# Optimization experiments

Hardware: AMD Instinct MI355X
Metric: run time of the kernel (lower is better)

## Reference

```python
import jax, jax.numpy as jnp
import numpy as np

HIDDEN = 896
NUM_Q_HEADS = 14
NUM_KV_HEADS = 2
HEAD_DIM = 64
ROPE_BASE = 10000.0
B, S = 4, 2048


def rotate_half(x):
    x1, x2 = jnp.split(x, 2, axis=-1)
    return jnp.concatenate((-x2, x1), axis=-1)


def rope_cos_sin(position_ids):
    # position_ids: [B, S] int -> cos/sin [B, 1, S, HEAD_DIM]
    inv_freq = 1.0 / (ROPE_BASE ** (jnp.arange(0, HEAD_DIM, 2, dtype=jnp.float32) / HEAD_DIM))
    freqs = position_ids.astype(jnp.float32)[..., None] * inv_freq  # [B,S,D/2]
    emb = jnp.concatenate((freqs, freqs), axis=-1)  # [B,S,D]
    return jnp.cos(emb)[:, None, :, :], jnp.sin(emb)[:, None, :, :]


def setup_inputs() -> dict:
    key = jax.random.key(0)
    k1, k2, k3, k4, k5 = jax.random.split(key, 5)
    s = 1.0 / np.sqrt(HIDDEN)
    return {
        "hidden_states": jax.random.normal(k1, (B, S, HIDDEN), dtype=jnp.float32),
        "position_ids": jnp.broadcast_to(jnp.arange(S, dtype=jnp.int64), (B, S)),
        "Wq": jax.random.normal(k2, (HIDDEN, NUM_Q_HEADS * HEAD_DIM), dtype=jnp.float32) * s,
        "Wk": jax.random.normal(k3, (HIDDEN, NUM_KV_HEADS * HEAD_DIM), dtype=jnp.float32) * s,
        "Wv": jax.random.normal(k4, (HIDDEN, NUM_KV_HEADS * HEAD_DIM), dtype=jnp.float32) * s,
        "Wo": jax.random.normal(k5, (NUM_Q_HEADS * HEAD_DIM, HIDDEN), dtype=jnp.float32) * s,
    }


def reference(hidden_states, position_ids, Wq, Wk, Wv, Wo):
    b, s, _ = hidden_states.shape
    n_rep = NUM_Q_HEADS // NUM_KV_HEADS

    q = (hidden_states @ Wq).reshape(b, s, NUM_Q_HEADS, HEAD_DIM).transpose(0, 2, 1, 3)   # [B,Hq,S,D]
    k = (hidden_states @ Wk).reshape(b, s, NUM_KV_HEADS, HEAD_DIM).transpose(0, 2, 1, 3)  # [B,Hkv,S,D]
    v = (hidden_states @ Wv).reshape(b, s, NUM_KV_HEADS, HEAD_DIM).transpose(0, 2, 1, 3)

    cos, sin = rope_cos_sin(position_ids)  # [B,1,S,D]
    q = q * cos + rotate_half(q) * sin
    k = k * cos + rotate_half(k) * sin

    # repeat_interleave KV heads to match query heads
    k = jnp.repeat(k, n_rep, axis=1)  # [B,Hq,S,D]
    v = jnp.repeat(v, n_rep, axis=1)

    scale = 1.0 / jnp.sqrt(jnp.float32(HEAD_DIM))
    attn = jnp.einsum('bhqd,bhkd->bhqk', q, k) * scale  # [B,Hq,S,S]
    attn = jax.nn.softmax(attn, axis=-1)
    out = jnp.einsum('bhqk,bhkd->bhqd', attn, v)  # [B,Hq,S,D]
    out = out.transpose(0, 2, 1, 3).reshape(b, s, NUM_Q_HEADS * HEAD_DIM)
    return out @ Wo
```

## Files before the change

### kernel.cpp

```cpp
#include <hip/hip_runtime.h>
#include <hip/hip_bf16.h>
#include <math.h>

typedef unsigned short ushort_t;
typedef __bf16 bf16x8 __attribute__((ext_vector_type(8)));
typedef float f32x4 __attribute__((ext_vector_type(4)));

#define HIDDEN 896
#define NQH 14
#define NKVH 2
#define HD 64
#define SEQ 2048
#define NBATCH 4

__device__ inline ushort_t f2bf(float x) {
  union { float f; unsigned u; } c; c.f = x;
  unsigned r = c.u + 0x7FFFu + ((c.u >> 16) & 1u);
  return (ushort_t)(r >> 16);
}

__device__ inline unsigned pack2bf(float a, float b) {
  union { float f; unsigned u; } ca, cb; ca.f = a; cb.f = b;
  unsigned ua = ca.u + 0x8000u, ub = cb.u + 0x8000u;
  return __builtin_amdgcn_perm(ub, ua, 0x07060302);
}

__device__ inline bf16x8 ldfrag(const ushort_t* p) {
  return *reinterpret_cast<const bf16x8*>(p);
}

__device__ inline void async16(const ushort_t* g, ushort_t* l) {
  __builtin_amdgcn_global_load_lds(
      (const __attribute__((address_space(1))) void*)g,
      (__attribute__((address_space(3))) void*)l, 16, 0, 0);
}


__device__ inline void transpose_sec(const float* __restrict__ in, ushort_t* __restrict__ out,
                                     int K, int N, int bx, int by) {
  __shared__ float tile[32][33];
  int k0 = by * 32, n0 = bx * 32;
  for (int r = threadIdx.y; r < 32; r += 8) {
    int k = k0 + r, n = n0 + threadIdx.x;
    tile[r][threadIdx.x] = (k < K && n < N) ? in[(size_t)k * N + n] : 0.f;
  }
  __syncthreads();
  for (int r = threadIdx.y; r < 32; r += 8) {
    int n = n0 + r, k = k0 + threadIdx.x;
    if (n < N && k < K) out[(size_t)n * K + k] = f2bf(tile[threadIdx.x][r]);
  }
}

__global__ void k_prep(const float* __restrict__ hidden, ushort_t* __restrict__ hb,
                       const float* __restrict__ Wq, const float* __restrict__ Wk,
                       const float* __restrict__ Wv, const float* __restrict__ Wo,
                       ushort_t* __restrict__ wT, ushort_t* __restrict__ woT,
                       float2* __restrict__ ctab) {
  const int blk = blockIdx.x;
  const int tid = threadIdx.y * 32 + threadIdx.x;
  if (blk < 7168) {
    int i = blk * 256 + tid;
    float4 v = reinterpret_cast<const float4*>(hidden)[i];
    ushort4 o;
    o.x = f2bf(v.x); o.y = f2bf(v.y); o.z = f2bf(v.z); o.w = f2bf(v.w);
    reinterpret_cast<ushort4*>(hb)[i] = o;
  } else if (blk < 7424) {
    int idx = (blk - 7168) * 256 + tid;
    int s = idx >> 5, dp = idx & 31;
    float inv = exp2f(-(float)dp * 0.41524101186092596f);
    float ang = (float)s * inv;
    float sn, cn;
    sincosf(ang, &sn, &cn);
    ctab[idx] = make_float2(cn, sn);
  } else if (blk < 8208) {
    int t = blk - 7424;
    transpose_sec(Wq, wT, 896, 896, t % 28, t / 28);
  } else if (blk < 8320) {
    int t = blk - 8208;
    transpose_sec(Wk, wT + (size_t)896 * 896, 896, 128, t % 4, t / 4);
  } else if (blk < 8432) {
    int t = blk - 8320;
    transpose_sec(Wv, wT + (size_t)1024 * 896, 896, 128, t % 4, t / 4);
  } else {
    int t = blk - 8432;
    transpose_sec(Wo, woT, 896, 896, t % 28, t / 28);
  }
}

__global__ __launch_bounds__(256) void k_qkv(
    const ushort_t* __restrict__ hb,
    const ushort_t* __restrict__ wT,
    const int* __restrict__ pos_ids,
    const float2* __restrict__ ctab,
    ushort_t* __restrict__ Qg,
    ushort_t* __restrict__ Kg,
    ushort_t* __restrict__ Vtg) {
  __shared__ ushort_t sa[128 * 32];
  __shared__ ushort_t sbb[128 * 32];

  const int f = blockIdx.x;
  const int x = f & 7, s8 = f >> 3;
  const int sect = s8 % 9;
  const int mt = (s8 / 9) * 8 + x;
  const int nt0 = sect * 128;
  const int m0 = mt * 128;
  const int tid = threadIdx.x;
  const int wave = tid >> 6, lane = tid & 63;
  const int l15 = lane & 15, quad = lane >> 4;
  const int wm = wave >> 1, wn = wave & 1;

  f32x4 acc[4][4];
  const f32x4 z4 = {0.f, 0.f, 0.f, 0.f};
#pragma unroll
  for (int a = 0; a < 4; ++a)
#pragma unroll
    for (int b = 0; b < 4; ++b) acc[a][b] = z4;

  for (int kt = 0; kt < 28; ++kt) {
    const int k0 = kt * 32;
    __syncthreads();
#pragma unroll
    for (int i = 0; i < 2; ++i) {
      int c = wave * 128 + i * 64 + lane;
      async16(hb + (size_t)(m0 + (c >> 2)) * HIDDEN + k0 + (c & 3) * 8,
              sa + (size_t)(wave * 128 + i * 64) * 8);
      async16(wT + (size_t)(nt0 + (c >> 2)) * HIDDEN + k0 + (c & 3) * 8,
              sbb + (size_t)(wave * 128 + i * 64) * 8);
    }
    __syncthreads();
    bf16x8 bf[4], af[4];
#pragma unroll
    for (int nb = 0; nb < 4; ++nb)
      bf[nb] = ldfrag(sbb + ((wn * 64 + nb * 16 + l15) * 32 + quad * 8));
#pragma unroll
    for (int mb = 0; mb < 4; ++mb)
      af[mb] = ldfrag(sa + ((wm * 64 + mb * 16 + l15) * 32 + quad * 8));
#pragma unroll
    for (int mb = 0; mb < 4; ++mb)
#pragma unroll
      for (int nb = 0; nb < 4; ++nb)
        acc[mb][nb] = __builtin_amdgcn_mfma_f32_16x16x32_bf16(af[mb], bf[nb], acc[mb][nb], 0, 0, 0);
  }

  if (sect < 8) {
    const bool isQ = sect < 7;
    const float csc = isQ ? 0.125f * 1.4426950408889634f : 1.0f;
    ushort_t* dst = isQ ? Qg : Kg;
    const int nheads = isQ ? NQH : NKVH;
    const int hh = isQ ? sect * 2 + wn : wn;
#pragma unroll
    for (int mb = 0; mb < 4; ++mb)
#pragma unroll
      for (int r = 0; r < 4; ++r) {
        int token = m0 + wm * 64 + mb * 16 + quad * 4 + r;
        int b = token >> 11, s = token & 2047;
        int pos = pos_ids[token];
        size_t base = ((size_t)(b * nheads + hh) * SEQ + s) * HD;
#pragma unroll
        for (int nb = 0; nb < 2; ++nb) {
          float2 cs = ctab[pos * 32 + nb * 16 + l15];
          float x0 = acc[mb][nb][r];
          float x1 = acc[mb][nb + 2][r];
          float y0 = (x0 * cs.x - x1 * cs.y) * csc;
          float y1 = (x1 * cs.x + x0 * cs.y) * csc;
          dst[base + nb * 16 + l15]      = f2bf(y0);
          dst[base + nb * 16 + l15 + 32] = f2bf(y1);
        }
      }
  } else {
#pragma unroll
    for (int mb = 0; mb < 4; ++mb) {
      int token0 = m0 + wm * 64 + mb * 16 + quad * 4;
      int b = token0 >> 11, s = token0 & 2047;
#pragma unroll
      for (int nb = 0; nb < 4; ++nb) {
        int d = nb * 16 + l15;
        uint2 pk;
        pk.x = pack2bf(acc[mb][nb][0], acc[mb][nb][1]);
        pk.y = pack2bf(acc[mb][nb][2], acc[mb][nb][3]);
        *reinterpret_cast<uint2*>(Vtg + ((size_t)(b * NKVH + wn) * HD + d) * SEQ + s) = pk;
      }
    }
  }
}

__global__ __launch_bounds__(256) void k_attn(
    const ushort_t* __restrict__ Qg,
    const ushort_t* __restrict__ Kg,
    const ushort_t* __restrict__ Vtg,
    ushort_t* __restrict__ attn) {
  __shared__ ushort_t kbuf[64 * 64];
  __shared__ ushort_t vbuf[64 * 64];
  __shared__ ushort_t pbuf[4][32 * 72];

  const int f = blockIdx.x;
  const int x = f & 7, s8 = f >> 3;
  const int lh = s8 >> 4;
  const int qt = s8 & 15;
  const int b = x >> 1, kvh = x & 1;
  const int h = kvh * 7 + lh;
  const int bh = b * NQH + h;
  const int tid = threadIdx.x;
  const int wave = tid >> 6, lane = tid & 63;
  const int l15 = lane & 15, quad = lane >> 4;
  const int q0 = qt * 128;

  bf16x8 qf[2][2];
#pragma unroll
  for (int qs = 0; qs < 2; ++qs) {
    const size_t qb = ((size_t)bh * SEQ + q0 + wave * 32 + qs * 16 + l15) * HD + quad * 8;
    qf[qs][0] = ldfrag(Qg + qb);
    qf[qs][1] = ldfrag(Qg + qb + 32);
  }

  bf16x8 ones;
#pragma unroll
  for (int i = 0; i < 8; ++i) ones[i] = (__bf16)1.0f;

  const size_t kbase = (size_t)(b * NKVH + kvh) * SEQ * HD;
  const size_t vbase = (size_t)(b * NKVH + kvh) * HD * SEQ;

  const int srow = tid >> 3;
  const int sc0 = (tid & 7) ^ (srow & 7);
  const int srow2 = (256 + tid) >> 3;
  const int sc2 = (tid & 7) ^ (srow2 & 7);
  const int sbase1 = wave * 64 * 8;
  const int sbase2 = (256 + wave * 64) * 8;

  f32x4 o[2][4];
  f32x4 lfr[2];
  const f32x4 z4 = {0.f, 0.f, 0.f, 0.f};
#pragma unroll
  for (int qs = 0; qs < 2; ++qs) {
    lfr[qs] = z4;
#pragma unroll
    for (int nb = 0; nb < 4; ++nb) o[qs][nb] = z4;
  }

  ushort_t* pw = pbuf[wave];

  for (int jt = 0; jt < 32; ++jt) {
    const int s0 = jt * 64;
    __syncthreads();
    async16(Kg + kbase + (size_t)(s0 + srow) * HD + sc0 * 8, kbuf + sbase1);
    async16(Vtg + vbase + (size_t)srow * SEQ + s0 + sc0 * 8, vbuf + sbase1);
    async16(Kg + kbase + (size_t)(s0 + srow2) * HD + sc2 * 8, kbuf + sbase2);
    async16(Vtg + vbase + (size_t)srow2 * SEQ + s0 + sc2 * 8, vbuf + sbase2);
    __syncthreads();

#pragma unroll
    for (int nb = 0; nb < 4; ++nb) {
      int row = nb * 16 + l15;
      int sw = row & 7;
      bf16x8 kf0 = ldfrag(kbuf + (row * 8 + (quad ^ sw)) * 8);
      bf16x8 kf1 = ldfrag(kbuf + (row * 8 + ((4 + quad) ^ sw)) * 8);
#pragma unroll
      for (int qs = 0; qs < 2; ++qs) {
        f32x4 t = z4;
        t = __builtin_amdgcn_mfma_f32_16x16x32_bf16(kf0, qf[qs][0], t, 0, 0, 0);
        t = __builtin_amdgcn_mfma_f32_16x16x32_bf16(kf1, qf[qs][1], t, 0, 0, 0);
        float p0 = __builtin_amdgcn_exp2f(t[0]);
        float p1 = __builtin_amdgcn_exp2f(t[1]);
        float p2 = __builtin_amdgcn_exp2f(t[2]);
        float p3 = __builtin_amdgcn_exp2f(t[3]);
        uint2 d;
        d.x = pack2bf(p0, p1);
        d.y = pack2bf(p2, p3);
        *reinterpret_cast<uint2*>(pw + (qs * 16 + l15) * 72 + nb * 16 + quad * 4) = d;
      }
    }

    bf16x8 pf[2][2];
#pragma unroll
    for (int qs = 0; qs < 2; ++qs) {
      pf[qs][0] = ldfrag(pw + (qs * 16 + l15) * 72 + quad * 8);
      pf[qs][1] = ldfrag(pw + (qs * 16 + l15) * 72 + 32 + quad * 8);
    }
#pragma unroll
    for (int qs = 0; qs < 2; ++qs) {
      lfr[qs] = __builtin_amdgcn_mfma_f32_16x16x32_bf16(pf[qs][0], ones, lfr[qs], 0, 0, 0);
      lfr[qs] = __builtin_amdgcn_mfma_f32_16x16x32_bf16(pf[qs][1], ones, lfr[qs], 0, 0, 0);
    }
#pragma unroll
    for (int nb = 0; nb < 4; ++nb) {
      int row = nb * 16 + l15;
      int sw = row & 7;
      bf16x8 vf0 = ldfrag(vbuf + (row * 8 + (quad ^ sw)) * 8);
      bf16x8 vf1 = ldfrag(vbuf + (row * 8 + ((4 + quad) ^ sw)) * 8);
#pragma unroll
      for (int qs = 0; qs < 2; ++qs) {
        o[qs][nb] = __builtin_amdgcn_mfma_f32_16x16x32_bf16(pf[qs][0], vf0, o[qs][nb], 0, 0, 0);
        o[qs][nb] = __builtin_amdgcn_mfma_f32_16x16x32_bf16(pf[qs][1], vf1, o[qs][nb], 0, 0, 0);
      }
    }
  }

#pragma unroll
  for (int qs = 0; qs < 2; ++qs) {
#pragma unroll
    for (int r = 0; r < 4; ++r) {
      float inv = 1.0f / lfr[qs][r];
      int qg = q0 + wave * 32 + qs * 16 + quad * 4 + r;
#pragma unroll
      for (int nb = 0; nb < 4; ++nb) {
        float val = o[qs][nb][r] * inv;
        attn[(size_t)(b * SEQ + qg) * (NQH * HD) + h * HD + nb * 16 + l15] = f2bf(val);
      }
    }
  }
}

__global__ __launch_bounds__(256) void k_oproj(
    const ushort_t* __restrict__ attn,
    const ushort_t* __restrict__ woT,
    float* __restrict__ out) {
  __shared__ ushort_t sa[128 * 32];
  __shared__ ushort_t sbb[128 * 32];

  const int f = blockIdx.x;
  const int x = f & 7, s8 = f >> 3;
  const int n_sect = s8 % 7;
  const int mt = (s8 / 7) * 8 + x;
  const int n0 = n_sect * 128;
  const int m0 = mt * 128;
  const int tid = threadIdx.x;
  const int wave = tid >> 6, lane = tid & 63;
  const int l15 = lane & 15, quad = lane >> 4;
  const int wm = wave >> 1, wn = wave & 1;

  f32x4 acc[4][4];
  const f32x4 z4 = {0.f, 0.f, 0.f, 0.f};
#pragma unroll
  for (int a = 0; a < 4; ++a)
#pragma unroll
    for (int b = 0; b < 4; ++b) acc[a][b] = z4;

  for (int kt = 0; kt < 28; ++kt) {
    const int k0 = kt * 32;
    __syncthreads();
#pragma unroll
    for (int i = 0; i < 2; ++i) {
      int c = wave * 128 + i * 64 + lane;
      async16(attn + (size_t)(m0 + (c >> 2)) * HIDDEN + k0 + (c & 3) * 8,
              sa + (size_t)(wave * 128 + i * 64) * 8);
      async16(woT + (size_t)(n0 + (c >> 2)) * HIDDEN + k0 + (c & 3) * 8,
              sbb + (size_t)(wave * 128 + i * 64) * 8);
    }
    __syncthreads();
    bf16x8 bf[4], af[4];
#pragma unroll
    for (int nb = 0; nb < 4; ++nb)
      bf[nb] = ldfrag(sbb + ((wn * 64 + nb * 16 + l15) * 32 + quad * 8));
#pragma unroll
    for (int mb = 0; mb < 4; ++mb)
      af[mb] = ldfrag(sa + ((wm * 64 + mb * 16 + l15) * 32 + quad * 8));
#pragma unroll
    for (int mb = 0; mb < 4; ++mb)
#pragma unroll
      for (int nb = 0; nb < 4; ++nb)
        acc[mb][nb] = __builtin_amdgcn_mfma_f32_16x16x32_bf16(af[mb], bf[nb], acc[mb][nb], 0, 0, 0);
  }

#pragma unroll
  for (int mb = 0; mb < 4; ++mb)
#pragma unroll
    for (int nb = 0; nb < 4; ++nb)
#pragma unroll
      for (int r = 0; r < 4; ++r)
        out[(size_t)(m0 + wm * 64 + mb * 16 + quad * 4 + r) * HIDDEN +
            n0 + wn * 64 + nb * 16 + l15] = acc[mb][nb][r];
}


extern "C" void kernel_launch(void* const* d_in, const int* in_sizes, int n_in,
                              void* d_out, int out_size, void* d_ws, size_t ws_size,
                              hipStream_t stream) {
  (void)in_sizes; (void)n_in; (void)out_size; (void)ws_size;
  const float* hidden = (const float*)d_in[0];
  const int* pos      = (const int*)d_in[1];
  const float* Wq     = (const float*)d_in[2];
  const float* Wk     = (const float*)d_in[3];
  const float* Wv     = (const float*)d_in[4];
  const float* Wo     = (const float*)d_in[5];
  float* out = (float*)d_out;

  char* ws = (char*)d_ws;
  ushort_t* hb   = (ushort_t*)(ws);
  ushort_t* wT   = (ushort_t*)(ws + 14680064);
  float2*   ctab = (float2*)  (ws + 16744448);
  ushort_t* Qg   = (ushort_t*)(ws + 17268736);
  ushort_t* Kg   = (ushort_t*)(ws + 31948800);
  ushort_t* Vtg  = (ushort_t*)(ws + 34045952);
  ushort_t* attn = (ushort_t*)(ws + 36143104);
  ushort_t* woT  = (ushort_t*)(ws + 50823168);

  k_prep<<<9216, dim3(32, 8), 0, stream>>>(hidden, hb, Wq, Wk, Wv, Wo, wT, woT, ctab);
  k_qkv<<<576, 256, 0, stream>>>(hb, wT, pos, ctab, Qg, Kg, Vtg);
  k_attn<<<896, 256, 0, stream>>>(Qg, Kg, Vtg, attn);
  k_oproj<<<448, 256, 0, stream>>>(attn, woT, out);
}
```

Measured before the change: 255.4 us.

## Widen GEMM K-tile with swizzled LDS, stage V transpose, enlarge attention query tile

Measured after the change: 277.4 us. +8.6%, slower.

```diff
diff --git a/kernel.cpp b/kernel.cpp
--- a/kernel.cpp
+++ b/kernel.cpp
@@ -95,8 +95,9 @@
     ushort_t* __restrict__ Qg,
     ushort_t* __restrict__ Kg,
     ushort_t* __restrict__ Vtg) {
-  __shared__ ushort_t sa[128 * 32];
-  __shared__ ushort_t sbb[128 * 32];
+  __shared__ ushort_t smem[16384];
+  ushort_t* sa = smem;
+  ushort_t* sbb = smem + 8192;
 
   const int f = blockIdx.x;
   const int x = f & 7, s8 = f >> 3;
@@ -108,6 +109,7 @@
   const int wave = tid >> 6, lane = tid & 63;
   const int l15 = lane & 15, quad = lane >> 4;
   const int wm = wave >> 1, wn = wave & 1;
+  const int sw = l15 & 7;
 
   f32x4 acc[4][4];
   const f32x4 z4 = {0.f, 0.f, 0.f, 0.f};
@@ -116,30 +118,37 @@
 #pragma unroll
     for (int b = 0; b < 4; ++b) acc[a][b] = z4;
 
-  for (int kt = 0; kt < 28; ++kt) {
-    const int k0 = kt * 32;
-    __syncthreads();
-#pragma unroll
-    for (int i = 0; i < 2; ++i) {
-      int c = wave * 128 + i * 64 + lane;
-      async16(hb + (size_t)(m0 + (c >> 2)) * HIDDEN + k0 + (c & 3) * 8,
-              sa + (size_t)(wave * 128 + i * 64) * 8);
-      async16(wT + (size_t)(nt0 + (c >> 2)) * HIDDEN + k0 + (c & 3) * 8,
-              sbb + (size_t)(wave * 128 + i * 64) * 8);
-    }
-    __syncthreads();
-    bf16x8 bf[4], af[4];
-#pragma unroll
-    for (int nb = 0; nb < 4; ++nb)
-      bf[nb] = ldfrag(sbb + ((wn * 64 + nb * 16 + l15) * 32 + quad * 8));
+  for (int kt = 0; kt < 14; ++kt) {
+    const int k0 = kt * 64;
+    __syncthreads();
+#pragma unroll
+    for (int i = 0; i < 4; ++i) {
+      int id = i * 256 + tid;
+      int row = id >> 3;
+      int cs = (id & 7) ^ (row & 7);
+      int base = (i * 256 + wave * 64) * 8;
+      async16(hb + (size_t)(m0 + row) * HIDDEN + k0 + cs * 8, sa + base);
+      async16(wT + (size_t)(nt0 + row) * HIDDEN + k0 + cs * 8, sbb + base);
+    }
+    __syncthreads();
+    bf16x8 af[4][2], bf[4][2];
+#pragma unroll
+    for (int kc = 0; kc < 2; ++kc) {
+      int c = kc * 4 + quad;
+#pragma unroll
+      for (int mb = 0; mb < 4; ++mb)
+        af[mb][kc] = ldfrag(sa + ((wm * 64 + mb * 16 + l15) * 8 + (c ^ sw)) * 8);
+#pragma unroll
+      for (int nb = 0; nb < 4; ++nb)
+        bf[nb][kc] = ldfrag(sbb + ((wn * 64 + nb * 16 + l15) * 8 + (c ^ sw)) * 8);
+    }
 #pragma unroll
     for (int mb = 0; mb < 4; ++mb)
-      af[mb] = ldfrag(sa + ((wm * 64 + mb * 16 + l15) * 32 + quad * 8));
-#pragma unroll
-    for (int mb = 0; mb < 4; ++mb)
-#pragma unroll
-      for (int nb = 0; nb < 4; ++nb)
-        acc[mb][nb] = __builtin_amdgcn_mfma_f32_16x16x32_bf16(af[mb], bf[nb], acc[mb][nb], 0, 0, 0);
+#pragma unroll
+      for (int nb = 0; nb < 4; ++nb) {
+        acc[mb][nb] = __builtin_amdgcn_mfma_f32_16x16x32_bf16(af[mb][0], bf[nb][0], acc[mb][nb], 0, 0, 0);
+        acc[mb][nb] = __builtin_amdgcn_mfma_f32_16x16x32_bf16(af[mb][1], bf[nb][1], acc[mb][nb], 0, 0, 0);
+      }
   }
 
   if (sect < 8) {
@@ -168,18 +177,31 @@
         }
       }
   } else {
+    __syncthreads();
+    ushort_t* vt = smem;
 #pragma unroll
     for (int mb = 0; mb < 4; ++mb) {
-      int token0 = m0 + wm * 64 + mb * 16 + quad * 4;
-      int b = token0 >> 11, s = token0 & 2047;
+      int tl = wm * 64 + mb * 16 + quad * 4;
+      int chunk = tl >> 3, ofs = tl & 7;
 #pragma unroll
       for (int nb = 0; nb < 4; ++nb) {
-        int d = nb * 16 + l15;
-        uint2 pk;
-        pk.x = pack2bf(acc[mb][nb][0], acc[mb][nb][1]);
-        pk.y = pack2bf(acc[mb][nb][2], acc[mb][nb][3]);
-        *reinterpret_cast<uint2*>(Vtg + ((size_t)(b * NKVH + wn) * HD + d) * SEQ + s) = pk;
-      }
+        int row = wn * 64 + nb * 16 + l15;
+        int slot = chunk ^ (row & 7);
+        ushort_t* p = vt + row * 128 + slot * 8 + ofs;
+        *reinterpret_cast<unsigned*>(p)     = pack2bf(acc[mb][nb][0], acc[mb][nb][1]);
+        *reinterpret_cast<unsigned*>(p + 2) = pack2bf(acc[mb][nb][2], acc[mb][nb][3]);
+      }
+    }
+    __syncthreads();
+    const int bb = m0 >> 11, s0 = m0 & 2047;
+#pragma unroll
+    for (int i = 0; i < 8; ++i) {
+      int id = i * 256 + tid;
+      int row = id >> 4, ch = id & 15;
+      int kvh = row >> 6, d = row & 63;
+      int slot = ch ^ (row & 7);
+      uint4 v = *reinterpret_cast<const uint4*>(vt + row * 128 + slot * 8);
+      *reinterpret_cast<uint4*>(Vtg + ((size_t)(bb * NKVH + kvh) * HD + d) * SEQ + s0 + ch * 8) = v;
     }
   }
 }
@@ -191,31 +213,28 @@
     ushort_t* __restrict__ attn) {
   __shared__ ushort_t kbuf[64 * 64];
   __shared__ ushort_t vbuf[64 * 64];
-  __shared__ ushort_t pbuf[4][32 * 72];
+  __shared__ ushort_t pbuf[4][64 * 72];
 
   const int f = blockIdx.x;
   const int x = f & 7, s8 = f >> 3;
-  const int lh = s8 >> 4;
-  const int qt = s8 & 15;
+  const int lh = s8 % 7;
+  const int qt = s8 / 7;
   const int b = x >> 1, kvh = x & 1;
   const int h = kvh * 7 + lh;
   const int bh = b * NQH + h;
   const int tid = threadIdx.x;
   const int wave = tid >> 6, lane = tid & 63;
   const int l15 = lane & 15, quad = lane >> 4;
-  const int q0 = qt * 128;
-
-  bf16x8 qf[2][2];
-#pragma unroll
-  for (int qs = 0; qs < 2; ++qs) {
-    const size_t qb = ((size_t)bh * SEQ + q0 + wave * 32 + qs * 16 + l15) * HD + quad * 8;
+  const int sw = l15 & 7;
+  const int q0 = qt * 256;
+
+  bf16x8 qf[4][2];
+#pragma unroll
+  for (int qs = 0; qs < 4; ++qs) {
+    const size_t qb = ((size_t)bh * SEQ + q0 + wave * 64 + qs * 16 + l15) * HD + quad * 8;
     qf[qs][0] = ldfrag(Qg + qb);
     qf[qs][1] = ldfrag(Qg + qb + 32);
   }
-
-  bf16x8 ones;
-#pragma unroll
-  for (int i = 0; i < 8; ++i) ones[i] = (__bf16)1.0f;
 
   const size_t kbase = (size_t)(b * NKVH + kvh) * SEQ * HD;
   const size_t vbase = (size_t)(b * NKVH + kvh) * HD * SEQ;
@@ -227,15 +246,13 @@
   const int sbase1 = wave * 64 * 8;
   const int sbase2 = (256 + wave * 64) * 8;
 
-  f32x4 o[2][4];
-  f32x4 lfr[2];
+  float lsum[4] = {0.f, 0.f, 0.f, 0.f};
+  f32x4 o[4][4];
   const f32x4 z4 = {0.f, 0.f, 0.f, 0.f};
 #pragma unroll
-  for (int qs = 0; qs < 2; ++qs) {
-    lfr[qs] = z4;
+  for (int qs = 0; qs < 4; ++qs)
 #pragma unroll
     for (int nb = 0; nb < 4; ++nb) o[qs][nb] = z4;
-  }
 
   ushort_t* pw = pbuf[wave];
 
@@ -251,11 +268,10 @@
 #pragma unroll
     for (int nb = 0; nb < 4; ++nb) {
       int row = nb * 16 + l15;
-      int sw = row & 7;
       bf16x8 kf0 = ldfrag(kbuf + (row * 8 + (quad ^ sw)) * 8);
       bf16x8 kf1 = ldfrag(kbuf + (row * 8 + ((4 + quad) ^ sw)) * 8);
 #pragma unroll
-      for (int qs = 0; qs < 2; ++qs) {
+      for (int qs = 0; qs < 4; ++qs) {
         f32x4 t = z4;
         t = __builtin_amdgcn_mfma_f32_16x16x32_bf16(kf0, qf[qs][0], t, 0, 0, 0);
         t = __builtin_amdgcn_mfma_f32_16x16x32_bf16(kf1, qf[qs][1], t, 0, 0, 0);
@@ -263,6 +279,7 @@
         float p1 = __builtin_amdgcn_exp2f(t[1]);
         float p2 = __builtin_amdgcn_exp2f(t[2]);
         float p3 = __builtin_amdgcn_exp2f(t[3]);
+        lsum[qs] += (p0 + p1) + (p2 + p3);
         uint2 d;
         d.x = pack2bf(p0, p1);
         d.y = pack2bf(p2, p3);
@@ -270,25 +287,19 @@
       }
     }
 
-    bf16x8 pf[2][2];
-#pragma unroll
-    for (int qs = 0; qs < 2; ++qs) {
+    bf16x8 pf[4][2];
+#pragma unroll
+    for (int qs = 0; qs < 4; ++qs) {
       pf[qs][0] = ldfrag(pw + (qs * 16 + l15) * 72 + quad * 8);
       pf[qs][1] = ldfrag(pw + (qs * 16 + l15) * 72 + 32 + quad * 8);
     }
 #pragma unroll
-    for (int qs = 0; qs < 2; ++qs) {
-      lfr[qs] = __builtin_amdgcn_mfma_f32_16x16x32_bf16(pf[qs][0], ones, lfr[qs], 0, 0, 0);
-      lfr[qs] = __builtin_amdgcn_mfma_f32_16x16x32_bf16(pf[qs][1], ones, lfr[qs], 0, 0, 0);
-    }
-#pragma unroll
     for (int nb = 0; nb < 4; ++nb) {
       int row = nb * 16 + l15;
-      int sw = row & 7;
       bf16x8 vf0 = ldfrag(vbuf + (row * 8 + (quad ^ sw)) * 8);
       bf16x8 vf1 = ldfrag(vbuf + (row * 8 + ((4 + quad) ^ sw)) * 8);
 #pragma unroll
-      for (int qs = 0; qs < 2; ++qs) {
+      for (int qs = 0; qs < 4; ++qs) {
         o[qs][nb] = __builtin_amdgcn_mfma_f32_16x16x32_bf16(pf[qs][0], vf0, o[qs][nb], 0, 0, 0);
         o[qs][nb] = __builtin_amdgcn_mfma_f32_16x16x32_bf16(pf[qs][1], vf1, o[qs][nb], 0, 0, 0);
       }
@@ -296,11 +307,19 @@
   }
 
 #pragma unroll
-  for (int qs = 0; qs < 2; ++qs) {
+  for (int qs = 0; qs < 4; ++qs) {
+    float s = lsum[qs];
+    s += __shfl_xor(s, 16);
+    s += __shfl_xor(s, 32);
+    lsum[qs] = 1.0f / s;
+  }
+
+#pragma unroll
+  for (int qs = 0; qs < 4; ++qs) {
 #pragma unroll
     for (int r = 0; r < 4; ++r) {
-      float inv = 1.0f / lfr[qs][r];
-      int qg = q0 + wave * 32 + qs * 16 + quad * 4 + r;
+      float inv = __shfl(lsum[qs], quad * 4 + r);
+      int qg = q0 + wave * 64 + qs * 16 + quad * 4 + r;
 #pragma unroll
       for (int nb = 0; nb < 4; ++nb) {
         float val = o[qs][nb][r] * inv;
@@ -314,8 +333,9 @@
     const ushort_t* __restrict__ attn,
     const ushort_t* __restrict__ woT,
     float* __restrict__ out) {
-  __shared__ ushort_t sa[128 * 32];
-  __shared__ ushort_t sbb[128 * 32];
+  __shared__ ushort_t smem[16384];
+  ushort_t* sa = smem;
+  ushort_t* sbb = smem + 8192;
 
   const int f = blockIdx.x;
   const int x = f & 7, s8 = f >> 3;
@@ -327,6 +347,7 @@
   const int wave = tid >> 6, lane = tid & 63;
   const int l15 = lane & 15, quad = lane >> 4;
   const int wm = wave >> 1, wn = wave & 1;
+  const int sw = l15 & 7;
 
   f32x4 acc[4][4];
   const f32x4 z4 = {0.f, 0.f, 0.f, 0.f};
@@ -335,30 +356,37 @@
 #pragma unroll
     for (int b = 0; b < 4; ++b) acc[a][b] = z4;
 
-  for (int kt = 0; kt < 28; ++kt) {
-    const int k0 = kt * 32;
-    __syncthreads();
-#pragma unroll
-    for (int i = 0; i < 2; ++i) {
-      int c = wave * 128 + i * 64 + lane;
-      async16(attn + (size_t)(m0 + (c >> 2)) * HIDDEN + k0 + (c & 3) * 8,
-              sa + (size_t)(wave * 128 + i * 64) * 8);
-      async16(woT + (size_t)(n0 + (c >> 2)) * HIDDEN + k0 + (c & 3) * 8,
-              sbb + (size_t)(wave * 128 + i * 64) * 8);
-    }
-    __syncthreads();
-    bf16x8 bf[4], af[4];
-#pragma unroll
-    for (int nb = 0; nb < 4; ++nb)
-      bf[nb] = ldfrag(sbb + ((wn * 64 + nb * 16 + l15) * 32 + quad * 8));
+  for (int kt = 0; kt < 14; ++kt) {
+    const int k0 = kt * 64;
+    __syncthreads();
+#pragma unroll
+    for (int i = 0; i < 4; ++i) {
+      int id = i * 256 + tid;
+      int row = id >> 3;
+      int cs = (id & 7) ^ (row & 7);
+      int base = (i * 256 + wave * 64) * 8;
+      async16(attn + (size_t)(m0 + row) * HIDDEN + k0 + cs * 8, sa + base);
+      async16(woT + (size_t)(n0 + row) * HIDDEN + k0 + cs * 8, sbb + base);
+    }
+    __syncthreads();
+    bf16x8 af[4][2], bf[4][2];
+#pragma unroll
+    for (int kc = 0; kc < 2; ++kc) {
+      int c = kc * 4 + quad;
+#pragma unroll
+      for (int mb = 0; mb < 4; ++mb)
+        af[mb][kc] = ldfrag(sa + ((wm * 64 + mb * 16 + l15) * 8 + (c ^ sw)) * 8);
+#pragma unroll
+      for (int nb = 0; nb < 4; ++nb)
+        bf[nb][kc] = ldfrag(sbb + ((wn * 64 + nb * 16 + l15) * 8 + (c ^ sw)) * 8);
+    }
 #pragma unroll
     for (int mb = 0; mb < 4; ++mb)
-      af[mb] = ldfrag(sa + ((wm * 64 + mb * 16 + l15) * 32 + quad * 8));
-#pragma unroll
-    for (int mb = 0; mb < 4; ++mb)
-#pragma unroll
-      for (int nb = 0; nb < 4; ++nb)
-        acc[mb][nb] = __builtin_amdgcn_mfma_f32_16x16x32_bf16(af[mb], bf[nb], acc[mb][nb], 0, 0, 0);
+#pragma unroll
+      for (int nb = 0; nb < 4; ++nb) {
+        acc[mb][nb] = __builtin_amdgcn_mfma_f32_16x16x32_bf16(af[mb][0], bf[nb][0], acc[mb][nb], 0, 0, 0);
+        acc[mb][nb] = __builtin_amdgcn_mfma_f32_16x16x32_bf16(af[mb][1], bf[nb][1], acc[mb][nb], 0, 0, 0);
+      }
   }
 
 #pragma unroll
@@ -396,6 +424,6 @@
 
   k_prep<<<9216, dim3(32, 8), 0, stream>>>(hidden, hb, Wq, Wk, Wv, Wo, wT, woT, ctab);
   k_qkv<<<576, 256, 0, stream>>>(hb, wT, pos, ctab, Qg, Kg, Vtg);
-  k_attn<<<896, 256, 0, stream>>>(Qg, Kg, Vtg, attn);
+  k_attn<<<448, 256, 0, stream>>>(Qg, Kg, Vtg, attn);
   k_oproj<<<448, 256, 0, stream>>>(attn, woT, out);
 }
```
